# Kernel optimization log

Measured on AMD Instinct MI355X. Metric: run time of the kernel, lower is better.

## Reference

```python
import jax, jax.numpy as jnp
import numpy as np

TEMPERATURE = 0.1
B, S, D, V = 4, 256, 768, 50257


def setup_inputs() -> dict:
    key = jax.random.key(0)
    k1, k2 = jax.random.split(key)
    return {
        "pred_embeds": jax.random.normal(k1, (B, S, D), dtype=jnp.float32),
        "embed_weight": jax.random.normal(k2, (V, D), dtype=jnp.float32),
    }


def reference(pred_embeds, embed_weight):
    # metric == 'l2': scores = -||p - t||^2, computed via the GEMM identity
    # -(||p||^2 + ||t||^2 - 2 p.t) instead of a (B,S,V,D) broadcast diff.
    p_sq = jnp.sum(pred_embeds * pred_embeds, axis=-1)        # (B,S)
    t_sq = jnp.sum(embed_weight * embed_weight, axis=-1)      # (V,)
    dot = jnp.einsum('bsd,vd->bsv', pred_embeds, embed_weight)  # (B,S,V)
    scores = 2.0 * dot - p_sq[..., None] - t_sq               # (B,S,V)

    softmax_pred_probs = jax.nn.softmax(scores / TEMPERATURE, axis=-1)
    predictions = jnp.argmax(softmax_pred_probs, axis=-1)      # (B,S) int

    # straight-through one-hot over probs
    y_hard = jax.nn.one_hot(predictions, V, dtype=softmax_pred_probs.dtype)
    pred_probs = y_hard - jax.lax.stop_gradient(softmax_pred_probs) + softmax_pred_probs

    # straight-through embedding lookup
    n_pred_embs = embed_weight[predictions]                    # (B,S,D)
    pred_embeds_st = pred_embeds + jax.lax.stop_gradient(n_pred_embs - pred_embeds)

    return (pred_embeds_st, pred_embeds, predictions, pred_probs, softmax_pred_probs)
```

## Files before the change

kernel.cpp:

```cpp
#include <hip/hip_runtime.h>
#include <math.h>

namespace {

constexpr int Bb = 4, Ss = 256, Dd = 768, Vv = 50257;
constexpr int Mm = Bb * Ss;
constexpr int BM = 128, BN = 128, BK = 32;
constexpr int NSTEP = Dd / BK;
constexpr int LDP = 40;
constexpr float SC = 14.4269504088896341f;

typedef _Float16 f16x8 __attribute__((ext_vector_type(8)));
typedef float f32x4 __attribute__((ext_vector_type(4)));

__global__ __launch_bounds__(256) void tsq_kernel(const float* __restrict__ W,
                                                  float* __restrict__ tsq) {
    int gid  = blockIdx.x * blockDim.x + threadIdx.x;
    int wave = gid >> 6;
    int lane = threadIdx.x & 63;
    if (wave >= Vv) return;
    const float4* row = reinterpret_cast<const float4*>(W + (size_t)wave * Dd);
    float s = 0.f;
#pragma unroll
    for (int i = 0; i < 3; ++i) {
        float4 v = row[lane + 64 * i];
        s = fmaf(v.x, v.x, s);
        s = fmaf(v.y, v.y, s);
        s = fmaf(v.z, v.z, s);
        s = fmaf(v.w, v.w, s);
    }
#pragma unroll
    for (int off = 32; off > 0; off >>= 1) s += __shfl_down(s, off);
    if (lane == 0) tsq[wave] = s;
}

__global__ __launch_bounds__(256) void gemm_kernel(const float* __restrict__ A,
                                                   const float* __restrict__ W,
                                                   const float* __restrict__ tsq,
                                                   float* __restrict__ scores) {
    __shared__ _Float16 Ah[BM][LDP];
    __shared__ _Float16 Al[BM][LDP];
    __shared__ _Float16 Wh[BN][LDP];
    __shared__ _Float16 Wl[BN][LDP];

    const int tid  = threadIdx.x;
    const int row0 = blockIdx.y * BM;
    const int col0 = blockIdx.x * BN;

    const int lr   = tid >> 1;
    const int lk   = (tid & 1) * 16;

    const int wid  = tid >> 6;
    const int lane = tid & 63;
    const int wr   = wid >> 1;
    const int wc   = wid & 1;
    const int fr   = lane & 15;
    const int fq   = lane >> 4;

    float4 ra[4], rw[4];
    const bool wvalid = (col0 + lr) < Vv;

    auto load_tiles = [&](int k0) {
        const float* ap = &A[(size_t)(row0 + lr) * Dd + k0 + lk];
        ra[0] = *reinterpret_cast<const float4*>(ap + 0);
        ra[1] = *reinterpret_cast<const float4*>(ap + 4);
        ra[2] = *reinterpret_cast<const float4*>(ap + 8);
        ra[3] = *reinterpret_cast<const float4*>(ap + 12);
        if (wvalid) {
            const float* wp = &W[(size_t)(col0 + lr) * Dd + k0 + lk];
            rw[0] = *reinterpret_cast<const float4*>(wp + 0);
            rw[1] = *reinterpret_cast<const float4*>(wp + 4);
            rw[2] = *reinterpret_cast<const float4*>(wp + 8);
            rw[3] = *reinterpret_cast<const float4*>(wp + 12);
        } else {
            rw[0] = rw[1] = rw[2] = rw[3] = make_float4(0.f, 0.f, 0.f, 0.f);
        }
    };

    auto store_tiles = [&]() {
        _Float16 hi[16], lo[16];
        const float* fa = reinterpret_cast<const float*>(ra);
#pragma unroll
        for (int i = 0; i < 16; ++i) {
            const float v = fa[i];
            const _Float16 h = (_Float16)v;
            hi[i] = h;
            lo[i] = (_Float16)(v - (float)h);
        }
        *reinterpret_cast<f16x8*>(&Ah[lr][lk])     = *reinterpret_cast<const f16x8*>(&hi[0]);
        *reinterpret_cast<f16x8*>(&Ah[lr][lk + 8]) = *reinterpret_cast<const f16x8*>(&hi[8]);
        *reinterpret_cast<f16x8*>(&Al[lr][lk])     = *reinterpret_cast<const f16x8*>(&lo[0]);
        *reinterpret_cast<f16x8*>(&Al[lr][lk + 8]) = *reinterpret_cast<const f16x8*>(&lo[8]);
        const float* fw = reinterpret_cast<const float*>(rw);
#pragma unroll
        for (int i = 0; i < 16; ++i) {
            const float v = fw[i];
            const _Float16 h = (_Float16)v;
            hi[i] = h;
            lo[i] = (_Float16)(v - (float)h);
        }
        *reinterpret_cast<f16x8*>(&Wh[lr][lk])     = *reinterpret_cast<const f16x8*>(&hi[0]);
        *reinterpret_cast<f16x8*>(&Wh[lr][lk + 8]) = *reinterpret_cast<const f16x8*>(&hi[8]);
        *reinterpret_cast<f16x8*>(&Wl[lr][lk])     = *reinterpret_cast<const f16x8*>(&lo[0]);
        *reinterpret_cast<f16x8*>(&Wl[lr][lk + 8]) = *reinterpret_cast<const f16x8*>(&lo[8]);
    };

    f32x4 acc[4][4];
#pragma unroll
    for (int m = 0; m < 4; ++m)
#pragma unroll
        for (int n = 0; n < 4; ++n) acc[m][n] = (f32x4){0.f, 0.f, 0.f, 0.f};

    load_tiles(0);
    for (int step = 0; step < NSTEP; ++step) {
        __syncthreads();
        store_tiles();
        __syncthreads();
        if (step + 1 < NSTEP) load_tiles((step + 1) * BK);

        f16x8 ah[4], al[4];
#pragma unroll
        for (int m = 0; m < 4; ++m) {
            const int r = wr * 64 + m * 16 + fr;
            ah[m] = *reinterpret_cast<const f16x8*>(&Ah[r][fq * 8]);
            al[m] = *reinterpret_cast<const f16x8*>(&Al[r][fq * 8]);
        }
#pragma unroll
        for (int n = 0; n < 4; ++n) {
            const int c = wc * 64 + n * 16 + fr;
            const f16x8 bh = *reinterpret_cast<const f16x8*>(&Wh[c][fq * 8]);
            const f16x8 bl = *reinterpret_cast<const f16x8*>(&Wl[c][fq * 8]);
#pragma unroll
            for (int m = 0; m < 4; ++m) {
                acc[m][n] = __builtin_amdgcn_mfma_f32_16x16x32_f16(ah[m], bh, acc[m][n], 0, 0, 0);
                acc[m][n] = __builtin_amdgcn_mfma_f32_16x16x32_f16(al[m], bh, acc[m][n], 0, 0, 0);
                acc[m][n] = __builtin_amdgcn_mfma_f32_16x16x32_f16(ah[m], bl, acc[m][n], 0, 0, 0);
            }
        }
    }

#pragma unroll
    for (int n = 0; n < 4; ++n) {
        const int gn = col0 + wc * 64 + n * 16 + fr;
        if (gn >= Vv) continue;
        const float t = tsq[gn];
#pragma unroll
        for (int m = 0; m < 4; ++m) {
            const int gm = row0 + wr * 64 + m * 16 + fq * 4;
#pragma unroll
            for (int r = 0; r < 4; ++r) {
                scores[(size_t)(gm + r) * Vv + gn] = fmaf(2.f, acc[m][n][r], -t);
            }
        }
    }
}

__global__ __launch_bounds__(256) void finalize_kernel(const float* __restrict__ A,
                                                       const float* __restrict__ W,
                                                       float* __restrict__ out0,
                                                       float* __restrict__ out1,
                                                       float* __restrict__ out2,
                                                       float* __restrict__ out3,
                                                       float* __restrict__ out4) {
    const int row = blockIdx.x;
    const int tid = threadIdx.x;
    float* srow = out4 + (size_t)row * Vv;
    float* hrow = out3 + (size_t)row * Vv;
    constexpr int NV4 = Vv >> 2;

    const float4* s4 = reinterpret_cast<const float4*>(srow);

    float m = -INFINITY;
    int   idx = 0;
    float sum = 0.f;
    for (int i = tid; i < NV4; i += 256) {
        const float4 v = s4[i];
        const float vv[4] = {v.x, v.y, v.z, v.w};
#pragma unroll
        for (int j = 0; j < 4; ++j) {
            const float val = vv[j];
            if (val > m) {
                sum *= exp2f((m - val) * SC);
                m = val;
                idx = 4 * i + j;
            }
            sum += exp2f((val - m) * SC);
        }
    }
    if (tid == 0) {
        const float val = srow[Vv - 1];
        if (val > m) { sum *= exp2f((m - val) * SC); m = val; idx = Vv - 1; }
        sum += exp2f((val - m) * SC);
    }

    __shared__ float smax[256];
    __shared__ int   sidx[256];
    __shared__ float ssum[256];
    smax[tid] = m; sidx[tid] = idx; ssum[tid] = sum;
    __syncthreads();
#pragma unroll
    for (int off = 128; off > 0; off >>= 1) {
        if (tid < off) {
            const float m1 = smax[tid], m2 = smax[tid + off];
            const int   i1 = sidx[tid], i2 = sidx[tid + off];
            const float s1 = ssum[tid], s2 = ssum[tid + off];
            if (m2 > m1 || (m2 == m1 && i2 < i1)) {
                smax[tid] = m2; sidx[tid] = i2;
                ssum[tid] = s1 * exp2f((m1 - m2) * SC) + s2;
            } else {
                ssum[tid] = s1 + s2 * exp2f((m2 - m1) * SC);
            }
        }
        __syncthreads();
    }
    const float gmax = smax[0];
    const int   pred = sidx[0];
    const float inv  = 1.0f / ssum[0];
    __syncthreads();

    float4* p4 = reinterpret_cast<float4*>(srow);
    float4* h4 = reinterpret_cast<float4*>(hrow);
    for (int i = tid; i < NV4; i += 256) {
        const float4 v = s4[i];
        const int b = 4 * i;
        float4 p, h;
        p.x = exp2f((v.x - gmax) * SC) * inv;
        p.y = exp2f((v.y - gmax) * SC) * inv;
        p.z = exp2f((v.z - gmax) * SC) * inv;
        p.w = exp2f((v.w - gmax) * SC) * inv;
        h.x = (b + 0 == pred) ? 1.f : 0.f;
        h.y = (b + 1 == pred) ? 1.f : 0.f;
        h.z = (b + 2 == pred) ? 1.f : 0.f;
        h.w = (b + 3 == pred) ? 1.f : 0.f;
        p4[i] = p;
        h4[i] = h;
    }
    if (tid == 0) {
        const float val = srow[Vv - 1];
        srow[Vv - 1] = exp2f((val - gmax) * SC) * inv;
        hrow[Vv - 1] = (pred == Vv - 1) ? 1.f : 0.f;
        out2[row] = (float)pred;
    }

    const float4* wrow = reinterpret_cast<const float4*>(W + (size_t)pred * Dd);
    const float4* arow = reinterpret_cast<const float4*>(A + (size_t)row * Dd);
    float4* o0 = reinterpret_cast<float4*>(out0 + (size_t)row * Dd);
    float4* o1 = reinterpret_cast<float4*>(out1 + (size_t)row * Dd);
    if (tid < Dd / 4) {
        o0[tid] = wrow[tid];
        o1[tid] = arow[tid];
    }
}

}

extern "C" void kernel_launch(void* const* d_in, const int* in_sizes, int n_in,
                              void* d_out, int out_size, void* d_ws, size_t ws_size,
                              hipStream_t stream) {
    const float* pred_embeds  = (const float*)d_in[0];
    const float* embed_weight = (const float*)d_in[1];

    float* out  = (float*)d_out;
    float* out0 = out;
    float* out1 = out0 + (size_t)Mm * Dd;
    float* out2 = out1 + (size_t)Mm * Dd;
    float* out3 = out2 + Mm;
    float* out4 = out3 + (size_t)Mm * Vv;

    float* tsq = (ws_size >= (size_t)Vv * sizeof(float)) ? (float*)d_ws : out3;

    tsq_kernel<<<(Vv + 3) / 4, 256, 0, stream>>>(embed_weight, tsq);

    dim3 grid((Vv + BN - 1) / BN, Mm / BM);
    gemm_kernel<<<grid, 256, 0, stream>>>(pred_embeds, embed_weight, tsq, out4);

    finalize_kernel<<<Mm, 256, 0, stream>>>(pred_embeds, embed_weight,
                                            out0, out1, out2, out3, out4);
}
```

Baseline: 523.2 us.

## Pre-split operands into packed fp16 hi/lo planes and load via global_load_lds

Adds a convert_pack kernel that splits A and W once into fp16 high and low parts, stored in a tile-contiguous layout in scratch space borrowed from the out3 buffer. The GEMM then copies these packed chunks straight into LDS with global_load_lds, so the per-tile conversion in registers and the register-staged prefetch are gone. The cost is an extra pass over W (about 150MB fp32 read and fp16 written) and no overlap of the next load with compute, since the loop now syncs before each chunk. It also relies on out3 being large enough to hold the packed planes and on finalize overwriting out3 afterwards.

```diff
diff --git a/kernel.cpp b/kernel.cpp
--- a/kernel.cpp
+++ b/kernel.cpp
@@ -6,12 +6,23 @@
 constexpr int Bb = 4, Ss = 256, Dd = 768, Vv = 50257;
 constexpr int Mm = Bb * Ss;
 constexpr int BM = 128, BN = 128, BK = 32;
-constexpr int NSTEP = Dd / BK;
-constexpr int LDP = 40;
+constexpr int NS = Dd / BK;
+constexpr int TW = (Vv + BN - 1) / BN;
+constexpr int TA = Mm / BM;
+constexpr int CHUNK = BM * BK;
 constexpr float SC = 14.4269504088896341f;
 
 typedef _Float16 f16x8 __attribute__((ext_vector_type(8)));
 typedef float f32x4 __attribute__((ext_vector_type(4)));
+
+constexpr size_t WPLANE = (size_t)TW * NS * CHUNK;
+constexpr size_t APLANE = (size_t)TA * NS * CHUNK;
+
+__device__ __forceinline__ void gload_lds16(const void* g, void* l) {
+    typedef __attribute__((address_space(3))) void lds_t;
+    typedef const __attribute__((address_space(1))) void gm_t;
+    __builtin_amdgcn_global_load_lds((gm_t*)g, (lds_t*)l, 16, 0, 0);
+}
 
 __global__ __launch_bounds__(256) void tsq_kernel(const float* __restrict__ W,
                                                   float* __restrict__ tsq) {
@@ -34,76 +45,68 @@
     if (lane == 0) tsq[wave] = s;
 }
 
-__global__ __launch_bounds__(256) void gemm_kernel(const float* __restrict__ A,
-                                                   const float* __restrict__ W,
+__global__ __launch_bounds__(256) void convert_pack(const float* __restrict__ src,
+                                                    _Float16* __restrict__ hp,
+                                                    _Float16* __restrict__ lp,
+                                                    int nrows) {
+    const int t    = blockIdx.x;
+    const int wid  = threadIdx.x >> 6;
+    const int lane = threadIdx.x & 63;
+    const int u    = blockIdx.y * 4 + wid;
+    const int s    = u >> 1;
+    const int half = u & 1;
+    const int r    = half * 64 + lane;
+    const int v    = t * BM + r;
+
+    float vals[32];
+    if (v < nrows) {
+        const float4* p = reinterpret_cast<const float4*>(src + (size_t)v * Dd + s * BK);
+#pragma unroll
+        for (int i = 0; i < 8; ++i) *reinterpret_cast<float4*>(&vals[4 * i]) = p[i];
+    } else {
+#pragma unroll
+        for (int i = 0; i < 32; ++i) vals[i] = 0.f;
+    }
+    const size_t chunk = ((size_t)t * NS + s) * CHUNK;
+#pragma unroll
+    for (int fq = 0; fq < 4; ++fq) {
+        _Float16 hi[8], lo[8];
+#pragma unroll
+        for (int e = 0; e < 8; ++e) {
+            const float x = vals[fq * 8 + e];
+            const _Float16 h = (_Float16)x;
+            hi[e] = h;
+            lo[e] = (_Float16)(x - (float)h);
+        }
+        *reinterpret_cast<f16x8*>(&hp[chunk + fq * (BM * 8) + (size_t)r * 8]) =
+            *reinterpret_cast<const f16x8*>(hi);
+        *reinterpret_cast<f16x8*>(&lp[chunk + fq * (BM * 8) + (size_t)r * 8]) =
+            *reinterpret_cast<const f16x8*>(lo);
+    }
+}
+
+__global__ __launch_bounds__(256) void gemm_kernel(const _Float16* __restrict__ Ahp,
+                                                   const _Float16* __restrict__ Alp,
+                                                   const _Float16* __restrict__ Whp,
+                                                   const _Float16* __restrict__ Wlp,
                                                    const float* __restrict__ tsq,
                                                    float* __restrict__ scores) {
-    __shared__ _Float16 Ah[BM][LDP];
-    __shared__ _Float16 Al[BM][LDP];
-    __shared__ _Float16 Wh[BN][LDP];
-    __shared__ _Float16 Wl[BN][LDP];
+    __shared__ _Float16 lds[4][CHUNK];
 
     const int tid  = threadIdx.x;
-    const int row0 = blockIdx.y * BM;
-    const int col0 = blockIdx.x * BN;
-
-    const int lr   = tid >> 1;
-    const int lk   = (tid & 1) * 16;
-
     const int wid  = tid >> 6;
     const int lane = tid & 63;
     const int wr   = wid >> 1;
     const int wc   = wid & 1;
     const int fr   = lane & 15;
     const int fq   = lane >> 4;
-
-    float4 ra[4], rw[4];
-    const bool wvalid = (col0 + lr) < Vv;
-
-    auto load_tiles = [&](int k0) {
-        const float* ap = &A[(size_t)(row0 + lr) * Dd + k0 + lk];
-        ra[0] = *reinterpret_cast<const float4*>(ap + 0);
-        ra[1] = *reinterpret_cast<const float4*>(ap + 4);
-        ra[2] = *reinterpret_cast<const float4*>(ap + 8);
-        ra[3] = *reinterpret_cast<const float4*>(ap + 12);
-        if (wvalid) {
-            const float* wp = &W[(size_t)(col0 + lr) * Dd + k0 + lk];
-            rw[0] = *reinterpret_cast<const float4*>(wp + 0);
-            rw[1] = *reinterpret_cast<const float4*>(wp + 4);
-            rw[2] = *reinterpret_cast<const float4*>(wp + 8);
-            rw[3] = *reinterpret_cast<const float4*>(wp + 12);
-        } else {
-            rw[0] = rw[1] = rw[2] = rw[3] = make_float4(0.f, 0.f, 0.f, 0.f);
-        }
-    };
-
-    auto store_tiles = [&]() {
-        _Float16 hi[16], lo[16];
-        const float* fa = reinterpret_cast<const float*>(ra);
-#pragma unroll
-        for (int i = 0; i < 16; ++i) {
-            const float v = fa[i];
-            const _Float16 h = (_Float16)v;
-            hi[i] = h;
-            lo[i] = (_Float16)(v - (float)h);
-        }
-        *reinterpret_cast<f16x8*>(&Ah[lr][lk])     = *reinterpret_cast<const f16x8*>(&hi[0]);
-        *reinterpret_cast<f16x8*>(&Ah[lr][lk + 8]) = *reinterpret_cast<const f16x8*>(&hi[8]);
-        *reinterpret_cast<f16x8*>(&Al[lr][lk])     = *reinterpret_cast<const f16x8*>(&lo[0]);
-        *reinterpret_cast<f16x8*>(&Al[lr][lk + 8]) = *reinterpret_cast<const f16x8*>(&lo[8]);
-        const float* fw = reinterpret_cast<const float*>(rw);
-#pragma unroll
-        for (int i = 0; i < 16; ++i) {
-            const float v = fw[i];
-            const _Float16 h = (_Float16)v;
-            hi[i] = h;
-            lo[i] = (_Float16)(v - (float)h);
-        }
-        *reinterpret_cast<f16x8*>(&Wh[lr][lk])     = *reinterpret_cast<const f16x8*>(&hi[0]);
-        *reinterpret_cast<f16x8*>(&Wh[lr][lk + 8]) = *reinterpret_cast<const f16x8*>(&hi[8]);
-        *reinterpret_cast<f16x8*>(&Wl[lr][lk])     = *reinterpret_cast<const f16x8*>(&lo[0]);
-        *reinterpret_cast<f16x8*>(&Wl[lr][lk + 8]) = *reinterpret_cast<const f16x8*>(&lo[8]);
-    };
+    const int tn   = blockIdx.x;
+    const int tm   = blockIdx.y;
+
+    const _Float16* gA_h = Ahp + (size_t)tm * NS * CHUNK;
+    const _Float16* gA_l = Alp + (size_t)tm * NS * CHUNK;
+    const _Float16* gW_h = Whp + (size_t)tn * NS * CHUNK;
+    const _Float16* gW_l = Wlp + (size_t)tn * NS * CHUNK;
 
     f32x4 acc[4][4];
 #pragma unroll
@@ -111,42 +114,49 @@
 #pragma unroll
         for (int n = 0; n < 4; ++n) acc[m][n] = (f32x4){0.f, 0.f, 0.f, 0.f};
 
-    load_tiles(0);
-    for (int step = 0; step < NSTEP; ++step) {
+    for (int s = 0; s < NS; ++s) {
+        if (s) __syncthreads();
+        const size_t so = (size_t)s * CHUNK;
+        const _Float16* gsrc[4] = {gA_h + so, gA_l + so, gW_h + so, gW_l + so};
+#pragma unroll
+        for (int c = 0; c < 4; ++c) {
+#pragma unroll
+            for (int i = 0; i < 2; ++i) {
+                const int seg = wid * 2 + i;
+                gload_lds16(gsrc[c] + seg * 512 + lane * 8, &lds[c][seg * 512]);
+            }
+        }
         __syncthreads();
-        store_tiles();
-        __syncthreads();
-        if (step + 1 < NSTEP) load_tiles((step + 1) * BK);
 
         f16x8 ah[4], al[4];
 #pragma unroll
         for (int m = 0; m < 4; ++m) {
             const int r = wr * 64 + m * 16 + fr;
-            ah[m] = *reinterpret_cast<const f16x8*>(&Ah[r][fq * 8]);
-            al[m] = *reinterpret_cast<const f16x8*>(&Al[r][fq * 8]);
+            ah[m] = *reinterpret_cast<const f16x8*>(&lds[0][fq * (BM * 8) + r * 8]);
+            al[m] = *reinterpret_cast<const f16x8*>(&lds[1][fq * (BM * 8) + r * 8]);
         }
 #pragma unroll
         for (int n = 0; n < 4; ++n) {
             const int c = wc * 64 + n * 16 + fr;
-            const f16x8 bh = *reinterpret_cast<const f16x8*>(&Wh[c][fq * 8]);
-            const f16x8 bl = *reinterpret_cast<const f16x8*>(&Wl[c][fq * 8]);
+            const f16x8 wh = *reinterpret_cast<const f16x8*>(&lds[2][fq * (BM * 8) + c * 8]);
+            const f16x8 wl = *reinterpret_cast<const f16x8*>(&lds[3][fq * (BM * 8) + c * 8]);
 #pragma unroll
             for (int m = 0; m < 4; ++m) {
-                acc[m][n] = __builtin_amdgcn_mfma_f32_16x16x32_f16(ah[m], bh, acc[m][n], 0, 0, 0);
-                acc[m][n] = __builtin_amdgcn_mfma_f32_16x16x32_f16(al[m], bh, acc[m][n], 0, 0, 0);
-                acc[m][n] = __builtin_amdgcn_mfma_f32_16x16x32_f16(ah[m], bl, acc[m][n], 0, 0, 0);
+                acc[m][n] = __builtin_amdgcn_mfma_f32_16x16x32_f16(ah[m], wh, acc[m][n], 0, 0, 0);
+                acc[m][n] = __builtin_amdgcn_mfma_f32_16x16x32_f16(al[m], wh, acc[m][n], 0, 0, 0);
+                acc[m][n] = __builtin_amdgcn_mfma_f32_16x16x32_f16(ah[m], wl, acc[m][n], 0, 0, 0);
             }
         }
     }
 
 #pragma unroll
     for (int n = 0; n < 4; ++n) {
-        const int gn = col0 + wc * 64 + n * 16 + fr;
+        const int gn = tn * BN + wc * 64 + n * 16 + fr;
         if (gn >= Vv) continue;
         const float t = tsq[gn];
 #pragma unroll
         for (int m = 0; m < 4; ++m) {
-            const int gm = row0 + wr * 64 + m * 16 + fq * 4;
+            const int gm = tm * BM + wr * 64 + m * 16 + fq * 4;
 #pragma unroll
             for (int r = 0; r < 4; ++r) {
                 scores[(size_t)(gm + r) * Vv + gn] = fmaf(2.f, acc[m][n][r], -t);
@@ -267,12 +277,17 @@
     float* out3 = out2 + Mm;
     float* out4 = out3 + (size_t)Mm * Vv;
 
-    float* tsq = (ws_size >= (size_t)Vv * sizeof(float)) ? (float*)d_ws : out3;
+    _Float16* Whp = (_Float16*)out3;
+    _Float16* Wlp = Whp + WPLANE;
+    _Float16* Ahp = Wlp + WPLANE;
+    _Float16* Alp = Ahp + APLANE;
+    float*    tsq = (float*)(Alp + APLANE);
 
     tsq_kernel<<<(Vv + 3) / 4, 256, 0, stream>>>(embed_weight, tsq);
-
-    dim3 grid((Vv + BN - 1) / BN, Mm / BM);
-    gemm_kernel<<<grid, 256, 0, stream>>>(pred_embeds, embed_weight, tsq, out4);
+    convert_pack<<<dim3(TW, 12), 256, 0, stream>>>(embed_weight, Whp, Wlp, Vv);
+    convert_pack<<<dim3(TA, 12), 256, 0, stream>>>(pred_embeds, Ahp, Alp, Mm);
+
+    gemm_kernel<<<dim3(TW, TA), 256, 0, stream>>>(Ahp, Alp, Whp, Wlp, tsq, out4);
 
     finalize_kernel<<<Mm, 256, 0, stream>>>(pred_embeds, embed_weight,
                                             out0, out1, out2, out3, out4);
```

New measurement: 549.6 us. 5.1% more time.
